# Optimization experiments

Measured on AMD Instinct MI355X. Metric: run time of the kernel, lower is better.

Reference implementation:

```python
import jax, jax.numpy as jnp
import numpy as np

B, T, D, H = 4, 2048, 1024, 16
HD = D // H
EPS = 1e-5


def gelu_tanh(x):
    c = jnp.sqrt(jnp.asarray(2.0 / jnp.pi, x.dtype))
    return 0.5 * x * (1.0 + jnp.tanh(c * (x + 0.044715 * x * x * x)))


def layernorm(x, gamma, beta):
    mean = jnp.mean(x, axis=-1, keepdims=True)
    var = jnp.var(x, axis=-1, keepdims=True)
    return gamma * (x - mean) / jnp.sqrt(var + EPS) + beta


def setup_inputs() -> dict:
    key = jax.random.key(0)
    ks = jax.random.split(key, 12)
    s = 0.02
    return {
        "x": jax.random.normal(ks[0], (B, T, D), jnp.float32),
        "Wq": jax.random.normal(ks[1], (D, D), jnp.float32) * s,
        "Wk": jax.random.normal(ks[2], (D, D), jnp.float32) * s,
        "Wv": jax.random.normal(ks[3], (D, D), jnp.float32) * s,
        "Wo": jax.random.normal(ks[4], (D, D), jnp.float32) * s,
        "bo": jnp.zeros((D,), jnp.float32),
        "W1": jax.random.normal(ks[5], (D, 4 * D), jnp.float32) * s,
        "b1": jnp.zeros((4 * D,), jnp.float32),
        "W2": jax.random.normal(ks[6], (4 * D, D), jnp.float32) * s,
        "b2": jnp.zeros((D,), jnp.float32),
        "gamma1": jnp.ones((D,), jnp.float32),
        "beta1": jnp.zeros((D,), jnp.float32),
        "gamma2": jnp.ones((D,), jnp.float32),
        "beta2": jnp.zeros((D,), jnp.float32),
    }


def reference(x, Wq, Wk, Wv, Wo, bo, W1, b1, W2, b2, gamma1, beta1, gamma2, beta2):
    # --- attention sublayer (pre-norm, causal) ---
    h = layernorm(x, gamma1, beta1)
    q = (h @ Wq).reshape(B, T, H, HD).transpose(0, 2, 1, 3)  # (B,H,T,hd)
    k = (h @ Wk).reshape(B, T, H, HD).transpose(0, 2, 1, 3)
    v = (h @ Wv).reshape(B, T, H, HD).transpose(0, 2, 1, 3)
    scores = jnp.einsum("bhqd,bhkd->bhqk", q, k) * (HD ** -0.5)
    causal = jnp.tril(jnp.ones((T, T), bool))
    scores = jnp.where(causal, scores, -jnp.inf)
    w = jax.nn.softmax(scores, axis=-1)
    attn = jnp.einsum("bhqk,bhkd->bhqd", w, v).transpose(0, 2, 1, 3).reshape(B, T, D)
    x = x + (attn @ Wo + bo)
    # --- FFN sublayer ---
    h2 = layernorm(x, gamma2, beta2)
    ff = gelu_tanh(h2 @ W1 + b1) @ W2 + b2
    return x + ff
```

## Files before the change

### kernel.cpp

```cpp
#include <hip/hip_runtime.h>
#include <hip/hip_bf16.h>


typedef __bf16 bf16;
typedef __attribute__((ext_vector_type(8))) __bf16 bf16x8;
typedef __attribute__((ext_vector_type(4))) __bf16 bf16x4;
typedef __attribute__((ext_vector_type(4))) float floatx4;

#define EXPC 0.18033688011112042f

__device__ __forceinline__ void async_cp16(const bf16* g, bf16* l) {
  __builtin_amdgcn_global_load_lds(
      (const __attribute__((address_space(1))) void*)g,
      (__attribute__((address_space(3))) void*)l, 16, 0, 0);
}

__global__ __launch_bounds__(256) void transpose_cvt4(
    const float* __restrict__ S0, const float* __restrict__ S1,
    const float* __restrict__ S2, const float* __restrict__ S3,
    bf16* __restrict__ D0, bf16* __restrict__ D1, bf16* __restrict__ D2,
    bf16* __restrict__ D3, int K, int N) {
  const float* W = (blockIdx.z == 0) ? S0 : (blockIdx.z == 1) ? S1
                   : (blockIdx.z == 2) ? S2 : S3;
  bf16* WT = (blockIdx.z == 0) ? D0 : (blockIdx.z == 1) ? D1
             : (blockIdx.z == 2) ? D2 : D3;
  __shared__ bf16 tile[32][33];
  const int tn = blockIdx.x;
  const int tk = blockIdx.y;
  const int t = threadIdx.x;
  const int row = t >> 3;
  const int c4 = (t & 7) * 4;

  const float* src = W + (size_t)(tk * 32 + row) * N + tn * 32 + c4;
  float4 v = *(const float4*)src;
  tile[row][c4 + 0] = (bf16)v.x;
  tile[row][c4 + 1] = (bf16)v.y;
  tile[row][c4 + 2] = (bf16)v.z;
  tile[row][c4 + 3] = (bf16)v.w;
  __syncthreads();
  bf16x4 o;
  o[0] = tile[c4 + 0][row];
  o[1] = tile[c4 + 1][row];
  o[2] = tile[c4 + 2][row];
  o[3] = tile[c4 + 3][row];
  *(bf16x4*)(WT + (size_t)(tn * 32 + row) * K + tk * 32 + c4) = o;
}

__global__ __launch_bounds__(256) void transpose_cvt(
    const float* __restrict__ W, bf16* __restrict__ WT, int K, int N) {
  __shared__ bf16 tile[32][33];
  const int tn = blockIdx.x;
  const int tk = blockIdx.y;
  const int t = threadIdx.x;
  const int row = t >> 3;
  const int c4 = (t & 7) * 4;

  const float* src = W + (size_t)(tk * 32 + row) * N + tn * 32 + c4;
  float4 v = *(const float4*)src;
  tile[row][c4 + 0] = (bf16)v.x;
  tile[row][c4 + 1] = (bf16)v.y;
  tile[row][c4 + 2] = (bf16)v.z;
  tile[row][c4 + 3] = (bf16)v.w;
  __syncthreads();
  bf16x4 o;
  o[0] = tile[c4 + 0][row];
  o[1] = tile[c4 + 1][row];
  o[2] = tile[c4 + 2][row];
  o[3] = tile[c4 + 3][row];
  *(bf16x4*)(WT + (size_t)(tn * 32 + row) * K + tk * 32 + c4) = o;
}

__global__ __launch_bounds__(256) void ln_kernel(
    const float* __restrict__ x, const float* __restrict__ gamma,
    const float* __restrict__ beta, bf16* __restrict__ out) {
  const int row = blockIdx.x;
  const int t = threadIdx.x;
  const float* xr = x + (size_t)row * 1024;
  float4 v4 = *(const float4*)(xr + t * 4);
  float a[4] = {v4.x, v4.y, v4.z, v4.w};
  float s = a[0] + a[1] + a[2] + a[3];
  float ss = a[0] * a[0] + a[1] * a[1] + a[2] * a[2] + a[3] * a[3];
  for (int off = 1; off < 64; off <<= 1) {
    s += __shfl_xor(s, off);
    ss += __shfl_xor(ss, off);
  }
  __shared__ float red[8];
  const int wid = t >> 6, lane = t & 63;
  if (lane == 0) { red[wid] = s; red[wid + 4] = ss; }
  __syncthreads();
  s = red[0] + red[1] + red[2] + red[3];
  ss = red[4] + red[5] + red[6] + red[7];
  const float mean = s * (1.0f / 1024.0f);
  const float var = ss * (1.0f / 1024.0f) - mean * mean;
  const float rstd = rsqrtf(var + 1e-5f);
  bf16x4 o;
  for (int j = 0; j < 4; ++j) {
    float g = gamma[t * 4 + j];
    float b = beta[t * 4 + j];
    o[j] = (bf16)((a[j] - mean) * rstd * g + b);
  }
  *(bf16x4*)(out + (size_t)row * 1024 + t * 4) = o;
}

__global__ __launch_bounds__(256) void init_resid_bias(
    const float* __restrict__ resid, const float* __restrict__ bias,
    float* __restrict__ out) {
  const size_t row = blockIdx.x;
  const int t = threadIdx.x;
  float4 r = *(const float4*)(resid + row * 1024 + t * 4);
  float4 b = *(const float4*)(bias + t * 4);
  r.x += b.x; r.y += b.y; r.z += b.z; r.w += b.w;
  *(float4*)(out + row * 1024 + t * 4) = r;
}

__device__ __forceinline__ float gelu_f(float x) {
  const float c = 0.7978845608028654f;
  float u = c * (x + 0.044715f * x * x * x);
  return 0.5f * x * (1.0f + tanhf(u));
}

template <int MODE>
__global__ __launch_bounds__(256, 2) void gemm_bt(
    const bf16* __restrict__ A, const bf16* __restrict__ BT,
    const float* __restrict__ bias, const float* __restrict__ resid,
    void* __restrict__ out, int M, int N, int K, int kChunk) {
  __shared__ bf16 sA[128 * 32];
  __shared__ bf16 sB[128 * 32];
  const int t = threadIdx.x;
  const int lane = t & 63, wid = t >> 6;
  const int waveM = wid >> 1, waveN = wid & 1;
  const int quad = lane >> 4, l16 = lane & 15;
  const size_t m0 = (size_t)blockIdx.x * 128;
  const size_t n0 = (size_t)blockIdx.y * 128;
  const int kBegin = blockIdx.z * kChunk;
  const int kEnd = kBegin + kChunk;

  floatx4 acc[4][4] = {};

  const int srow = wid * 16 + (lane >> 2);
  const int scol = (lane & 3) * 8;
  const bf16* Ag = A + (m0 + srow) * (size_t)K + scol;
  const bf16* Bg = BT + (n0 + srow) * (size_t)K + scol;
  bf16* sAp = sA + wid * 512 + lane * 8;
  bf16* sBp = sB + wid * 512 + lane * 8;

  for (int k0 = kBegin; k0 < kEnd; k0 += 32) {
    __syncthreads();
    async_cp16(Ag + k0, sAp);
    async_cp16(Ag + (size_t)64 * K + k0, sAp + 64 * 32);
    async_cp16(Bg + k0, sBp);
    async_cp16(Bg + (size_t)64 * K + k0, sBp + 64 * 32);
    __syncthreads();
    bf16x8 af[4], bfv[4];
#pragma unroll
    for (int i = 0; i < 4; ++i)
      af[i] = *(const bf16x8*)&sA[(waveM * 64 + i * 16 + l16) * 32 + quad * 8];
#pragma unroll
    for (int i = 0; i < 4; ++i)
      bfv[i] = *(const bf16x8*)&sB[(waveN * 64 + i * 16 + l16) * 32 + quad * 8];
#pragma unroll
    for (int mt = 0; mt < 4; ++mt)
#pragma unroll
      for (int nt = 0; nt < 4; ++nt)
        acc[mt][nt] = __builtin_amdgcn_mfma_f32_16x16x32_bf16(
            af[mt], bfv[nt], acc[mt][nt], 0, 0, 0);
  }

#pragma unroll
  for (int mt = 0; mt < 4; ++mt) {
#pragma unroll
    for (int nt = 0; nt < 4; ++nt) {
      const size_t row_base = m0 + waveM * 64 + mt * 16 + quad * 4;
      const size_t col = n0 + waveN * 64 + nt * 16 + l16;
#pragma unroll
      for (int r = 0; r < 4; ++r) {
        const size_t row = row_base + r;
        float v = acc[mt][nt][r];
        if (MODE == 1) {
          v = gelu_f(v + bias[col]);
          ((bf16*)out)[row * N + col] = (bf16)v;
        } else if (MODE == 2) {
          v += bias[col] + resid[row * N + col];
          ((float*)out)[row * N + col] = v;
        } else if (MODE == 4) {
          atomicAdd(&((float*)out)[row * N + col], v);
        } else {
          ((bf16*)out)[row * N + col] = (bf16)v;
        }
      }
    }
  }
}

__global__ __launch_bounds__(256) void attn_kernel(
    const bf16* __restrict__ QKV, bf16* __restrict__ O) {
  const int idx = blockIdx.x;
  const int qt = 31 - (idx >> 6);
  const int bh = idx & 63;
  const int b = bh >> 4, h = bh & 15;
  const int t = threadIdx.x;
  const int lane = t & 63, wid = t >> 6;
  const int quad = lane >> 4, l16 = lane & 15;

  __shared__ bf16 sQ[64][72];
  __shared__ bf16 sK[64][72];
  __shared__ bf16 sVt[64][72];
  __shared__ bf16 sP[4][16][72];

  const size_t qbase = (size_t)b * 2048 * 3072 + (size_t)h * 64;
  const size_t kbase = qbase + 1024;
  const size_t vbase = qbase + 2048;
  const int q0 = qt * 64;

  for (int c = t; c < 512; c += 256) {
    int row = c >> 3, sub = (c & 7) * 8;
    *(bf16x8*)&sQ[row][sub] =
        *(const bf16x8*)(QKV + qbase + (size_t)(q0 + row) * 3072 + sub);
  }
  __syncthreads();

  bf16x8 aq[2];
  aq[0] = *(const bf16x8*)&sQ[wid * 16 + l16][quad * 8];
  aq[1] = *(const bf16x8*)&sQ[wid * 16 + l16][32 + quad * 8];

  float l_part[4] = {0.f, 0.f, 0.f, 0.f};
  floatx4 o_acc[4] = {};

  for (int kt = 0; kt <= qt; ++kt) {
    __syncthreads();
    const int k0 = kt * 64;
    for (int c = t; c < 512; c += 256) {
      int row = c >> 3, sub = (c & 7) * 8;
      *(bf16x8*)&sK[row][sub] =
          *(const bf16x8*)(QKV + kbase + (size_t)(k0 + row) * 3072 + sub);
      bf16x8 v8 = *(const bf16x8*)(QKV + vbase + (size_t)(k0 + row) * 3072 + sub);
#pragma unroll
      for (int j = 0; j < 8; ++j)
        sVt[sub + j][row ^ (sub & 56)] = v8[j];
    }
    __syncthreads();

    float p[4][4];
#pragma unroll
    for (int nt = 0; nt < 4; ++nt) {
      floatx4 acc = {};
#pragma unroll
      for (int ks = 0; ks < 2; ++ks) {
        bf16x8 bk = *(const bf16x8*)&sK[nt * 16 + l16][ks * 32 + quad * 8];
        acc = __builtin_amdgcn_mfma_f32_16x16x32_bf16(aq[ks], bk, acc, 0, 0, 0);
      }
#pragma unroll
      for (int r = 0; r < 4; ++r) p[nt][r] = exp2f(acc[r] * EXPC);
    }

    if (kt == qt) {
      const int qrow_base = q0 + wid * 16 + quad * 4;
#pragma unroll
      for (int nt = 0; nt < 4; ++nt) {
        const int kk = k0 + nt * 16 + l16;
#pragma unroll
        for (int r = 0; r < 4; ++r)
          if (kk > qrow_base + r) p[nt][r] = 0.f;
      }
    }

#pragma unroll
    for (int nt = 0; nt < 4; ++nt)
#pragma unroll
      for (int r = 0; r < 4; ++r) {
        l_part[r] += p[nt][r];
        sP[wid][quad * 4 + r][nt * 16 + l16] = (bf16)p[nt][r];
      }

    bf16x8 ap[2];
    ap[0] = *(const bf16x8*)&sP[wid][l16][quad * 8];
    ap[1] = *(const bf16x8*)&sP[wid][l16][32 + quad * 8];
#pragma unroll
    for (int nt = 0; nt < 4; ++nt) {
      const int r2 = nt * 16 + l16;
#pragma unroll
      for (int ks = 0; ks < 2; ++ks) {
        bf16x8 bv =
            *(const bf16x8*)&sVt[r2][(ks * 32 + quad * 8) ^ (r2 & 56)];
        o_acc[nt] =
            __builtin_amdgcn_mfma_f32_16x16x32_bf16(ap[ks], bv, o_acc[nt], 0, 0, 0);
      }
    }
  }

#pragma unroll
  for (int off = 1; off < 16; off <<= 1)
#pragma unroll
    for (int r = 0; r < 4; ++r) l_part[r] += __shfl_xor(l_part[r], off);
  float inv[4];
#pragma unroll
  for (int r = 0; r < 4; ++r) inv[r] = 1.0f / l_part[r];

#pragma unroll
  for (int nt = 0; nt < 4; ++nt)
#pragma unroll
    for (int r = 0; r < 4; ++r) {
      const size_t row = (size_t)b * 2048 + q0 + wid * 16 + quad * 4 + r;
      const size_t col = (size_t)h * 64 + nt * 16 + l16;
      O[row * 1024 + col] = (bf16)(o_acc[nt][r] * inv[r]);
    }
}

extern "C" void kernel_launch(void* const* d_in, const int* in_sizes, int n_in,
                              void* d_out, int out_size, void* d_ws, size_t ws_size,
                              hipStream_t stream) {
  const float* x = (const float*)d_in[0];
  const float* Wq = (const float*)d_in[1];
  const float* Wk = (const float*)d_in[2];
  const float* Wv = (const float*)d_in[3];
  const float* Wo = (const float*)d_in[4];
  const float* bo = (const float*)d_in[5];
  const float* W1 = (const float*)d_in[6];
  const float* b1 = (const float*)d_in[7];
  const float* W2 = (const float*)d_in[8];
  const float* b2 = (const float*)d_in[9];
  const float* gamma1 = (const float*)d_in[10];
  const float* beta1 = (const float*)d_in[11];
  const float* gamma2 = (const float*)d_in[12];
  const float* beta2 = (const float*)d_in[13];

  char* ws = (char*)d_ws;
  const size_t MB = (size_t)1 << 20;
  bf16* WqkvT = (bf16*)(ws + 0 * MB);
  bf16* WoT = (bf16*)(ws + 6 * MB);
  bf16* W1T = (bf16*)(ws + 8 * MB);
  bf16* W2T = (bf16*)(ws + 16 * MB);
  bf16* h1  = (bf16*)(ws + 24 * MB);
  bf16* QKVb = (bf16*)(ws + 40 * MB);
  bf16* attnb = (bf16*)(ws + 88 * MB);
  float* x1 = (float*)(ws + 104 * MB);
  bf16* h2  = (bf16*)(ws + 136 * MB);
  bf16* midb = (bf16*)(ws + 152 * MB);

  dim3 blk(256);

  transpose_cvt4<<<dim3(32, 32, 4), blk, 0, stream>>>(
      Wq, Wk, Wv, Wo, WqkvT, WqkvT + (size_t)1024 * 1024,
      WqkvT + (size_t)2048 * 1024, WoT, 1024, 1024);
  transpose_cvt<<<dim3(128, 32), blk, 0, stream>>>(W1, W1T, 1024, 4096);
  transpose_cvt<<<dim3(32, 128), blk, 0, stream>>>(W2, W2T, 4096, 1024);

  ln_kernel<<<8192, blk, 0, stream>>>(x, gamma1, beta1, h1);

  gemm_bt<3><<<dim3(64, 24), blk, 0, stream>>>(h1, WqkvT, nullptr, nullptr,
                                               QKVb, 8192, 3072, 1024, 1024);

  attn_kernel<<<dim3(2048), blk, 0, stream>>>(QKVb, attnb);

  gemm_bt<2><<<dim3(64, 8), blk, 0, stream>>>(attnb, WoT, bo, x, x1,
                                              8192, 1024, 1024, 1024);

  ln_kernel<<<8192, blk, 0, stream>>>(x1, gamma2, beta2, h2);

  gemm_bt<1><<<dim3(64, 32), blk, 0, stream>>>(h2, W1T, b1, nullptr, midb,
                                               8192, 4096, 1024, 1024);

  init_resid_bias<<<8192, blk, 0, stream>>>(x1, b2, (float*)d_out);
  gemm_bt<4><<<dim3(64, 8, 2), blk, 0, stream>>>(midb, W2T, nullptr, nullptr,
                                                 d_out, 8192, 1024, 4096, 2048);
}
```

Measured before the change: 565.6 us.

## Template GEMM K-tile with XOR-swizzled LDS and drop split-K atomics for W2

Adds a compile-time BK parameter to the bf16 GEMM, with an XOR swizzle of the LDS layout for BK>=64 to avoid bank conflicts, and runs several MFMA k-steps per barrier pair. The N=1024 GEMMs (Wo and W2) now use BK=128 so each tile sync covers more compute. The split-K atomicAdd path for the FFN down-projection and its separate resid+bias init kernel are replaced by one non-split GEMM with a fused bias+residual epilogue. In exchange that GEMM runs only 512 blocks, half the previous parallelism, and the larger tiles raise LDS use to 64KB per block, which may limit occupancy.

```diff
diff --git a/kernel.cpp b/kernel.cpp
--- a/kernel.cpp
+++ b/kernel.cpp
@@ -102,68 +102,67 @@
   *(bf16x4*)(out + (size_t)row * 1024 + t * 4) = o;
 }
 
-__global__ __launch_bounds__(256) void init_resid_bias(
-    const float* __restrict__ resid, const float* __restrict__ bias,
-    float* __restrict__ out) {
-  const size_t row = blockIdx.x;
-  const int t = threadIdx.x;
-  float4 r = *(const float4*)(resid + row * 1024 + t * 4);
-  float4 b = *(const float4*)(bias + t * 4);
-  r.x += b.x; r.y += b.y; r.z += b.z; r.w += b.w;
-  *(float4*)(out + row * 1024 + t * 4) = r;
-}
-
 __device__ __forceinline__ float gelu_f(float x) {
   const float c = 0.7978845608028654f;
   float u = c * (x + 0.044715f * x * x * x);
   return 0.5f * x * (1.0f + tanhf(u));
 }
 
-template <int MODE>
+template <int MODE, int BK>
 __global__ __launch_bounds__(256, 2) void gemm_bt(
     const bf16* __restrict__ A, const bf16* __restrict__ BT,
     const float* __restrict__ bias, const float* __restrict__ resid,
-    void* __restrict__ out, int M, int N, int K, int kChunk) {
-  __shared__ bf16 sA[128 * 32];
-  __shared__ bf16 sB[128 * 32];
+    void* __restrict__ out, int M, int N, int K) {
+  __shared__ bf16 sA[128 * BK];
+  __shared__ bf16 sB[128 * BK];
+  constexpr int GPR = BK / 8;
+  constexpr int CPT = GPR / 2;
+  constexpr int RPI = 256 / GPR;
+  constexpr int SW = (BK >= 64) ? 7 : 0;
+
   const int t = threadIdx.x;
   const int lane = t & 63, wid = t >> 6;
   const int waveM = wid >> 1, waveN = wid & 1;
   const int quad = lane >> 4, l16 = lane & 15;
   const size_t m0 = (size_t)blockIdx.x * 128;
   const size_t n0 = (size_t)blockIdx.y * 128;
-  const int kBegin = blockIdx.z * kChunk;
-  const int kEnd = kBegin + kChunk;
 
   floatx4 acc[4][4] = {};
 
-  const int srow = wid * 16 + (lane >> 2);
-  const int scol = (lane & 3) * 8;
-  const bf16* Ag = A + (m0 + srow) * (size_t)K + scol;
-  const bf16* Bg = BT + (n0 + srow) * (size_t)K + scol;
-  bf16* sAp = sA + wid * 512 + lane * 8;
-  bf16* sBp = sB + wid * 512 + lane * 8;
-
-  for (int k0 = kBegin; k0 < kEnd; k0 += 32) {
+  const int r0 = t / GPR;
+  const int gp = t % GPR;
+  const int gsrc = gp ^ (r0 & SW);
+  const bf16* Ag = A + (m0 + r0) * (size_t)K + gsrc * 8;
+  const bf16* Bg = BT + (n0 + r0) * (size_t)K + gsrc * 8;
+  bf16* sAp = sA + t * 8;
+  bf16* sBp = sB + t * 8;
+
+  for (int k0 = 0; k0 < K; k0 += BK) {
     __syncthreads();
-    async_cp16(Ag + k0, sAp);
-    async_cp16(Ag + (size_t)64 * K + k0, sAp + 64 * 32);
-    async_cp16(Bg + k0, sBp);
-    async_cp16(Bg + (size_t)64 * K + k0, sBp + 64 * 32);
+#pragma unroll
+    for (int it = 0; it < CPT; ++it) {
+      async_cp16(Ag + k0 + (size_t)(it * RPI) * K, sAp + it * 2048);
+      async_cp16(Bg + k0 + (size_t)(it * RPI) * K, sBp + it * 2048);
+    }
     __syncthreads();
-    bf16x8 af[4], bfv[4];
-#pragma unroll
-    for (int i = 0; i < 4; ++i)
-      af[i] = *(const bf16x8*)&sA[(waveM * 64 + i * 16 + l16) * 32 + quad * 8];
-#pragma unroll
-    for (int i = 0; i < 4; ++i)
-      bfv[i] = *(const bf16x8*)&sB[(waveN * 64 + i * 16 + l16) * 32 + quad * 8];
-#pragma unroll
-    for (int mt = 0; mt < 4; ++mt)
-#pragma unroll
-      for (int nt = 0; nt < 4; ++nt)
-        acc[mt][nt] = __builtin_amdgcn_mfma_f32_16x16x32_bf16(
-            af[mt], bfv[nt], acc[mt][nt], 0, 0, 0);
+#pragma unroll
+    for (int ks = 0; ks < BK / 32; ++ks) {
+      bf16x8 af[4], bfv[4];
+#pragma unroll
+      for (int i = 0; i < 4; ++i) {
+        const int rowA = waveM * 64 + i * 16 + l16;
+        const int g = ((ks * 4 + quad) ^ (l16 & SW)) * 8;
+        af[i] = *(const bf16x8*)&sA[rowA * BK + g];
+        const int rowB = waveN * 64 + i * 16 + l16;
+        bfv[i] = *(const bf16x8*)&sB[rowB * BK + g];
+      }
+#pragma unroll
+      for (int mt = 0; mt < 4; ++mt)
+#pragma unroll
+        for (int nt = 0; nt < 4; ++nt)
+          acc[mt][nt] = __builtin_amdgcn_mfma_f32_16x16x32_bf16(
+              af[mt], bfv[nt], acc[mt][nt], 0, 0, 0);
+    }
   }
 
 #pragma unroll
@@ -182,8 +181,6 @@
         } else if (MODE == 2) {
           v += bias[col] + resid[row * N + col];
           ((float*)out)[row * N + col] = v;
-        } else if (MODE == 4) {
-          atomicAdd(&((float*)out)[row * N + col], v);
         } else {
           ((bf16*)out)[row * N + col] = (bf16)v;
         }
@@ -347,20 +344,19 @@
 
   ln_kernel<<<8192, blk, 0, stream>>>(x, gamma1, beta1, h1);
 
-  gemm_bt<3><<<dim3(64, 24), blk, 0, stream>>>(h1, WqkvT, nullptr, nullptr,
-                                               QKVb, 8192, 3072, 1024, 1024);
+  gemm_bt<3, 32><<<dim3(64, 24), blk, 0, stream>>>(h1, WqkvT, nullptr, nullptr,
+                                                   QKVb, 8192, 3072, 1024);
 
   attn_kernel<<<dim3(2048), blk, 0, stream>>>(QKVb, attnb);
 
-  gemm_bt<2><<<dim3(64, 8), blk, 0, stream>>>(attnb, WoT, bo, x, x1,
-                                              8192, 1024, 1024, 1024);
+  gemm_bt<2, 128><<<dim3(64, 8), blk, 0, stream>>>(attnb, WoT, bo, x, x1,
+                                                   8192, 1024, 1024);
 
   ln_kernel<<<8192, blk, 0, stream>>>(x1, gamma2, beta2, h2);
 
-  gemm_bt<1><<<dim3(64, 32), blk, 0, stream>>>(h2, W1T, b1, nullptr, midb,
-                                               8192, 4096, 1024, 1024);
-
-  init_resid_bias<<<8192, blk, 0, stream>>>(x1, b2, (float*)d_out);
-  gemm_bt<4><<<dim3(64, 8, 2), blk, 0, stream>>>(midb, W2T, nullptr, nullptr,
-                                                 d_out, 8192, 1024, 4096, 2048);
-}
+  gemm_bt<1, 32><<<dim3(64, 32), blk, 0, stream>>>(h2, W1T, b1, nullptr, midb,
+                                                   8192, 4096, 1024);
+
+  gemm_bt<2, 128><<<dim3(64, 8), blk, 0, stream>>>(midb, W2T, b2, x1, d_out,
+                                                   8192, 1024, 4096);
+}
```

After: 496.6 us. 12.2% less time.
